# Kernel optimization log

Hardware: AMD Instinct MI355X
Metric: run time of the kernel (lower is better)

Reference implementation:

```python
import jax, jax.numpy as jnp
import numpy as np

ALPHA = 0.2      # LeakyReLU negative slope
NEG = -9e15     # mask fill value, as in pyGAT

B, N, NFEAT, NHID, NCLASS, NHEADS = 4, 2048, 128, 64, 32, 8


def setup_inputs() -> dict:
    key = jax.random.key(0)
    ks = jax.random.split(key, 8)
    x = jax.random.normal(ks[0], (B, N, NFEAT), dtype=jnp.float32)
    adj = jax.random.randint(ks[1], (B, N, N), 0, 2, dtype=jnp.int32)
    W = jax.random.normal(ks[2], (NHEADS, NFEAT, NHID), dtype=jnp.float32) * 0.1
    a1 = jax.random.normal(ks[3], (NHEADS, NHID), dtype=jnp.float32) * 0.1
    a2 = jax.random.normal(ks[4], (NHEADS, NHID), dtype=jnp.float32) * 0.1
    Wo = jax.random.normal(ks[5], (NHEADS * NHID, NCLASS), dtype=jnp.float32) * 0.1
    ao1 = jax.random.normal(ks[6], (NCLASS,), dtype=jnp.float32) * 0.1
    ao2 = jax.random.normal(ks[7], (NCLASS,), dtype=jnp.float32) * 0.1
    return {"x": x, "adj": adj, "W": W, "a1": a1, "a2": a2,
            "Wo": Wo, "ao1": ao1, "ao2": ao2}


def _gat_forward(x, adj, W, a1, a2, Wo, ao1, ao2):
    mask = adj > 0  # [B, N, N]
    # --- multi-head layer (concat=True) ---
    Wh = jnp.einsum('bnf,hfd->bhnd', x, W)          # [B,H,N,nhid]
    f1 = jnp.einsum('bhnd,hd->bhn', Wh, a1)          # Wh @ a[:nhid]
    f2 = jnp.einsum('bhnd,hd->bhn', Wh, a2)          # Wh @ a[nhid:]
    e = jax.nn.leaky_relu(f1[..., :, None] + f2[..., None, :], ALPHA)
    att = jax.nn.softmax(jnp.where(mask[:, None], e, NEG), axis=-1)
    h = jax.nn.elu(jnp.einsum('bhnm,bhmd->bhnd', att, Wh))  # [B,H,N,nhid]
    # torch.cat along dim=2: [B, N, H*nhid]
    h = jnp.transpose(h, (0, 2, 1, 3)).reshape(B, N, NHEADS * NHID)
    # (dropout layers are no-ops in eval mode)
    # --- output head (concat=False, no ELU) ---
    Wh2 = jnp.einsum('bnf,fc->bnc', h, Wo)           # [B,N,nclass]
    g1 = jnp.einsum('bnc,c->bn', Wh2, ao1)
    g2 = jnp.einsum('bnc,c->bn', Wh2, ao2)
    e2 = jax.nn.leaky_relu(g1[:, :, None] + g2[:, None, :], ALPHA)
    att2 = jax.nn.softmax(jnp.where(mask, e2, NEG), axis=-1)
    return jnp.einsum('bnm,bmc->bnc', att2, Wh2)     # [B,N,nclass]


def reference(x, adj, W, a1, a2, Wo, ao1, ao2):
    return _gat_forward(x, adj, W, a1, a2, Wo, ao1, ao2)
```

## Files before the change

kernel.cpp:

```cpp
#include <hip/hip_runtime.h>


typedef _Float16 half8  __attribute__((ext_vector_type(8)));
typedef _Float16 half2_ __attribute__((ext_vector_type(2)));
typedef float  float4_ __attribute__((ext_vector_type(4)));
typedef unsigned int uint4_ __attribute__((ext_vector_type(4)));

#if __has_builtin(__builtin_amdgcn_exp2f)
#define EXP2(x) __builtin_amdgcn_exp2f(x)
#else
#define EXP2(x) __expf((x) * 0.69314718055994531f)
#endif
#define LOG2E 1.44269504088896340f

static __device__ __forceinline__ unsigned pkh(float a, float b) {
#if __has_builtin(__builtin_amdgcn_cvt_pkrtz)
  return __builtin_bit_cast(unsigned, __builtin_amdgcn_cvt_pkrtz(a, b));
#else
  half2_ h = {(_Float16)a, (_Float16)b};
  return __builtin_bit_cast(unsigned, h);
#endif
}
static __device__ __forceinline__ unsigned short f2h(float f) {
  _Float16 h = (_Float16)f;
  return __builtin_bit_cast(unsigned short, h);
}

static __device__ __forceinline__ unsigned bitm(unsigned mb, int jj) {
#if __has_builtin(__builtin_amdgcn_sbfe)
  return (unsigned)__builtin_amdgcn_sbfe((int)mb, jj, 1);
#else
  return 0u - ((mb >> jj) & 1u);
#endif
}
static __device__ __forceinline__ unsigned pmask(unsigned s0, unsigned s1) {
  return __builtin_amdgcn_perm(s1, s0, 0x05040100u);
}
static __device__ __forceinline__ unsigned wmaxh(unsigned u, unsigned u2,
    unsigned pm, half2_ Ah, half2_ A2h) {
  half2_ p = Ah * __builtin_bit_cast(half2_, u);
  half2_ n = A2h * __builtin_bit_cast(half2_, u2);
  half2_ m = __builtin_elementwise_max(p, n);
  return __builtin_bit_cast(unsigned, m) & pm;
}

__global__ __launch_bounds__(256) void k_wfrag(
    const float* __restrict__ Wm, const float* __restrict__ Wo,
    unsigned short* __restrict__ Wf, unsigned short* __restrict__ WoF) {
  if (blockIdx.x < 32) {
    const int T = blockIdx.x * 256 + threadIdx.x;
    const int lane = T & 63;
    int r = T >> 6;
    const int nt = r & 3; r >>= 2;
    const int kstep = r & 3; r >>= 2;
    const int h = r;
    const int kk = kstep * 32 + (lane >> 4) * 8;
    const int n = nt * 16 + (lane & 15);
    const float* sp = Wm + h * 8192 + kk * 64 + n;
    unsigned short o[8];
    #pragma unroll
    for (int jj = 0; jj < 8; ++jj) o[jj] = f2h(sp[jj * 64]);
    *(uint4_*)(Wf + T * 8) = *(uint4_*)o;
  } else {
    const int T = (blockIdx.x - 32) * 256 + threadIdx.x;
    const int lane = T & 63;
    const int nt = (T >> 6) & 1, kstep = T >> 7;
    const int kk = kstep * 32 + (lane >> 4) * 8;
    const int n = nt * 16 + (lane & 15);
    unsigned short o[8];
    #pragma unroll
    for (int jj = 0; jj < 8; ++jj) o[jj] = f2h(Wo[(kk + jj) * 32 + n]);
    *(uint4_*)(WoF + T * 8) = *(uint4_*)o;
  }
}

__global__ __launch_bounds__(256) void k_front(
    const int* __restrict__ adj, unsigned long long* __restrict__ maskb,
    const float* __restrict__ x, const unsigned short* __restrict__ Wf,
    const float* __restrict__ a1, const float* __restrict__ a2,
    unsigned short* __restrict__ WhF, float* __restrict__ f1,
    unsigned short* __restrict__ Uv, unsigned short* __restrict__ U2v) {
  __shared__ float wsm[64 * 68];
  const int bx = blockIdx.x;
  const int t = threadIdx.x;
  if (bx >= 1024) {
    const int lane = t & 63, wid = t >> 6;
    const int s = lane & 15;
    const long long row0 = (long long)(bx - 1024) * 4;
    for (int rr = 0; rr < 4; ++rr) {
      const long long row = row0 + rr;
      const int4* src = (const int4*)(adj + row * 2048);
      #pragma unroll
      for (int c = 0; c < 2; ++c) {
        int4 v = src[c * 256 + t];
        unsigned nib = (v.x != 0 ? 1u : 0u) | (v.y != 0 ? 2u : 0u) |
                       (v.z != 0 ? 4u : 0u) | (v.w != 0 ? 8u : 0u);
        unsigned lo = (s < 8) ? (nib << (s * 4)) : 0u;
        unsigned hi = (s >= 8) ? (nib << ((s - 8) * 4)) : 0u;
        #pragma unroll
        for (int off = 1; off < 16; off <<= 1) {
          lo |= __shfl_xor(lo, off);
          hi |= __shfl_xor(hi, off);
        }
        if (s == 0) {
          const int word = c * 16 + wid * 4 + (lane >> 4);
          maskb[(((row >> 11) * 32 + word) << 11) + (row & 2047)] =
              ((unsigned long long)hi << 32) | (unsigned long long)lo;
        }
      }
    }
    return;
  }
  const int itile = bx & 31, bh = bx >> 5;
  const int b = bh >> 3, h = bh & 7;
  const int i0 = itile * 64;
  const int lane = t & 63, w = t >> 6;
  const int cl = lane & 15, q = lane >> 4;
  const float* xrow = x + ((long long)b * 2048 + i0 + w * 16 + cl) * 128;
  const unsigned short* wfh = Wf + h * 8192;
  float4_ acc0 = {0.f, 0.f, 0.f, 0.f}, acc1 = acc0, acc2 = acc0, acc3 = acc0;
  #pragma unroll
  for (int kstep = 0; kstep < 4; ++kstep) {
    const float* xp = xrow + kstep * 32 + q * 8;
    const float4 xa = *(const float4*)xp;
    const float4 xb = *(const float4*)(xp + 4);
    uint4_ ap;
    ap.x = pkh(xa.x, xa.y);
    ap.y = pkh(xa.z, xa.w);
    ap.z = pkh(xb.x, xb.y);
    ap.w = pkh(xb.z, xb.w);
    const half8 af = __builtin_bit_cast(half8, ap);
    const unsigned short* bp = wfh + kstep * 2048 + lane * 8;
    const half8 b0 = *(const half8*)(bp);
    const half8 b1 = *(const half8*)(bp + 512);
    const half8 b2 = *(const half8*)(bp + 1024);
    const half8 b3 = *(const half8*)(bp + 1536);
    acc0 = __builtin_amdgcn_mfma_f32_16x16x32_f16(af, b0, acc0, 0, 0, 0);
    acc1 = __builtin_amdgcn_mfma_f32_16x16x32_f16(af, b1, acc1, 0, 0, 0);
    acc2 = __builtin_amdgcn_mfma_f32_16x16x32_f16(af, b2, acc2, 0, 0, 0);
    acc3 = __builtin_amdgcn_mfma_f32_16x16x32_f16(af, b3, acc3, 0, 0, 0);
  }
  {
    float4_ accs[4] = {acc0, acc1, acc2, acc3};
    #pragma unroll
    for (int nt = 0; nt < 4; ++nt)
      #pragma unroll
      for (int reg = 0; reg < 4; ++reg)
        wsm[(w * 16 + q * 4 + reg) * 68 + nt * 16 + cl] = accs[nt][reg];
  }
  __syncthreads();
  {
    const int row = t >> 2, seg = t & 3;
    const float* wr = wsm + row * 68 + seg * 16;
    const float4* a1p = (const float4*)(a1 + h * 64 + seg * 16);
    const float4* a2p = (const float4*)(a2 + h * 64 + seg * 16);
    float p1 = 0.f, p2 = 0.f;
    #pragma unroll
    for (int u = 0; u < 4; ++u) {
      const float4 wv = *(const float4*)(wr + u * 4);
      const float4 v1 = a1p[u];
      const float4 v2 = a2p[u];
      p1 += wv.x * v1.x + wv.y * v1.y + wv.z * v1.z + wv.w * v1.w;
      p2 += wv.x * v2.x + wv.y * v2.y + wv.z * v2.z + wv.w * v2.w;
    }
    p1 += __shfl_xor(p1, 1); p1 += __shfl_xor(p1, 2);
    p2 += __shfl_xor(p2, 1); p2 += __shfl_xor(p2, 2);
    if (seg == 0) {
      f1[(long long)bh * 2048 + i0 + row] = p1 * LOG2E;
      const float s2 = p2 * LOG2E;
      Uv[(long long)bh * 2048 + i0 + row] = f2h(EXP2(s2));
      U2v[(long long)bh * 2048 + i0 + row] = f2h(EXP2(0.2f * s2));
    }
  }
  #pragma unroll
  for (int u = 0; u < 2; ++u) {
    const int idx = u * 256 + t;
    const int l2 = idx & 63, nt2 = (idx >> 6) & 3, ks2 = idx >> 8;
    const int jrow = ks2 * 32 + (l2 >> 4) * 8;
    const int d = nt2 * 16 + (l2 & 15);
    uint4_ o;
    o.x = pkh(wsm[(jrow + 0) * 68 + d], wsm[(jrow + 1) * 68 + d]);
    o.y = pkh(wsm[(jrow + 2) * 68 + d], wsm[(jrow + 3) * 68 + d]);
    o.z = pkh(wsm[(jrow + 4) * 68 + d], wsm[(jrow + 5) * 68 + d]);
    o.w = pkh(wsm[(jrow + 6) * 68 + d], wsm[(jrow + 7) * 68 + d]);
    const long long off = (long long)bh * 131072 + (long long)itile * 4096 +
                          ks2 * 2048 + nt2 * 512 + l2 * 8;
    *(uint4_*)(WhF + off) = o;
  }
}

__global__ __launch_bounds__(256) void k_attn1(
    const unsigned short* __restrict__ whf, const float* __restrict__ f1v,
    const unsigned short* __restrict__ Uv, const unsigned short* __restrict__ U2v,
    const unsigned long long* __restrict__ maskb, unsigned short* __restrict__ hA) {
  __shared__ __align__(16) unsigned short bsm[2][8192];
  const int bh = blockIdx.y, b = bh >> 3, hh = bh & 7;
  const int t = threadIdx.x;
  const int lane = t & 63, wid = t >> 6;
  const int cl = lane & 15, q = lane >> 4, qs = q * 8;
  const long long i_g = (long long)blockIdx.x * 64 + wid * 16 + cl;
  const float f1i = f1v[(long long)bh * 2048 + i_g];
  const float A = EXP2(f1i), A2 = EXP2(0.2f * f1i);
  const half2_ Ah = __builtin_bit_cast(half2_, pkh(A, A));
  const half2_ A2h = __builtin_bit_cast(half2_, pkh(A2, A2));
  const uint2* mT = (const uint2*)maskb;
  const long long mbase = (long long)b * 65536 + i_g;
  const unsigned short* whfb = whf + (long long)bh * 131072;
  const unsigned short* Ub  = Uv  + (long long)bh * 2048;
  const unsigned short* U2b = U2v + (long long)bh * 2048;
  const float4* gB = (const float4*)whfb;
  const half8 vones = {1.0f16, 1.0f16, 1.0f16, 1.0f16, 1.0f16, 1.0f16, 1.0f16, 1.0f16};
  {
    const float4 s0 = gB[t], s1 = gB[256 + t], s2 = gB[512 + t], s3 = gB[768 + t];
    float4* dp = (float4*)bsm[0] + t;
    dp[0] = s0; dp[256] = s1; dp[512] = s2; dp[768] = s3;
  }
  uint2 mw0_c = mT[mbase], mw1_c = mT[mbase + 2048];
  float4_ acc0 = {0.f, 0.f, 0.f, 0.f}, acc1 = acc0, acc2 = acc0, acc3 = acc0;
  float4_ accz = acc0;
  for (int s = 0; s < 16; ++s) {
    __syncthreads();
    const int sn = (s < 15) ? (s + 1) : 15;
    const float4* gp = gB + sn * 1024 + t;
    const float4 stn0 = gp[0], stn1 = gp[256], stn2 = gp[512], stn3 = gp[768];
    const uint2 mwA = mw0_c, mwB = mw1_c;
    mw0_c = mT[mbase + (long long)(sn * 2) * 2048];
    mw1_c = mT[mbase + (long long)(sn * 2 + 1) * 2048];
    const unsigned short* bsb = bsm[s & 1] + lane * 8;
    #pragma unroll
    for (int jc2 = 0; jc2 < 2; ++jc2) {
      const int jc = s * 2 + jc2;
      const uint2 mw = jc2 ? mwB : mwA;
      #pragma unroll
      for (int ks = 0; ks < 2; ++ks) {
        const uint4_ uv  = *(const uint4_*)(Ub  + jc * 64 + ks * 32 + qs);
        const uint4_ u2v = *(const uint4_*)(U2b + jc * 64 + ks * 32 + qs);
        const unsigned mb = (ks ? mw.y : mw.x) >> qs;
        const unsigned s0 = bitm(mb, 0), s1 = bitm(mb, 1), s2 = bitm(mb, 2),
                       s3 = bitm(mb, 3), s4 = bitm(mb, 4), s5 = bitm(mb, 5),
                       s6 = bitm(mb, 6), s7 = bitm(mb, 7);
        uint4_ pk;
        pk.x = wmaxh(uv.x, u2v.x, pmask(s0, s1), Ah, A2h);
        pk.y = wmaxh(uv.y, u2v.y, pmask(s2, s3), Ah, A2h);
        pk.z = wmaxh(uv.z, u2v.z, pmask(s4, s5), Ah, A2h);
        pk.w = wmaxh(uv.w, u2v.w, pmask(s6, s7), Ah, A2h);
        const half8 af = __builtin_bit_cast(half8, pk);
        const unsigned short* bp = bsb + (jc2 * 2 + ks) * 2048;
        const half8 b0 = *(const half8*)(bp);
        const half8 b1 = *(const half8*)(bp + 512);
        const half8 b2 = *(const half8*)(bp + 1024);
        const half8 b3 = *(const half8*)(bp + 1536);
        acc0 = __builtin_amdgcn_mfma_f32_16x16x32_f16(af, b0, acc0, 0, 0, 0);
        acc1 = __builtin_amdgcn_mfma_f32_16x16x32_f16(af, b1, acc1, 0, 0, 0);
        acc2 = __builtin_amdgcn_mfma_f32_16x16x32_f16(af, b2, acc2, 0, 0, 0);
        acc3 = __builtin_amdgcn_mfma_f32_16x16x32_f16(af, b3, acc3, 0, 0, 0);
        accz = __builtin_amdgcn_mfma_f32_16x16x32_f16(af, vones, accz, 0, 0, 0);
      }
    }
    if (s < 15) {
      float4* dp = (float4*)bsm[(s + 1) & 1] + t;
      dp[0] = stn0; dp[256] = stn1; dp[512] = stn2; dp[768] = stn3;
    }
  }
  __syncthreads();
  float* hs = (float*)bsm;
  {
    float4_ accs[4] = {acc0, acc1, acc2, acc3};
    #pragma unroll
    for (int reg = 0; reg < 4; ++reg) {
      const float rz = 1.f / accz[reg];
      #pragma unroll
      for (int nt = 0; nt < 4; ++nt) {
        float v = accs[nt][reg] * rz;
        v = (v > 0.f) ? v : (__expf(v) - 1.f);
        hs[(wid * 16 + q * 4 + reg) * 68 + nt * 16 + cl] = v;
      }
    }
  }
  __syncthreads();
  const int rtg0 = b * 128 + blockIdx.x * 4;
  #pragma unroll
  for (int u = 0; u < 2; ++u) {
    const int id = u * 256 + t;
    const int l2 = id & 63, ks2 = (id >> 6) & 1, rtile = id >> 7;
    const int rowl = rtile * 16 + (l2 & 15);
    const int d = ks2 * 32 + (l2 >> 4) * 8;
    const float* hp = hs + rowl * 68 + d;
    uint4_ o;
    o.x = pkh(hp[0], hp[1]); o.y = pkh(hp[2], hp[3]);
    o.z = pkh(hp[4], hp[5]); o.w = pkh(hp[6], hp[7]);
    const long long rt = rtg0 + rtile;
    const int kstep = hh * 2 + ks2;
    *(uint4_*)(hA + ((rt * 16 + kstep) * 64 + l2) * 8) = o;
  }
}

__global__ __launch_bounds__(128) void k_ogemm(
    const unsigned short* __restrict__ hA, const unsigned short* __restrict__ WoF,
    const float* __restrict__ ao1, const float* __restrict__ ao2,
    unsigned short* __restrict__ Wh2F, float* __restrict__ g1,
    unsigned short* __restrict__ gU, unsigned short* __restrict__ gU2) {
  __shared__ float w2s[32 * 36];
  const int t = threadIdx.x, lane = t & 63, wv = t >> 6;
  const int cl = lane & 15, q = lane >> 4;
  const long long rt = (long long)blockIdx.x * 2 + wv;
  float4_ acc0 = {0.f, 0.f, 0.f, 0.f}, acc1 = acc0;
  const unsigned short* ap = hA + rt * 8192 + lane * 8;
  const unsigned short* bp = WoF + lane * 8;
  #pragma unroll
  for (int kstep = 0; kstep < 16; ++kstep) {
    const half8 af = *(const half8*)(ap + kstep * 512);
    const half8 b0 = *(const half8*)(bp + kstep * 1024);
    const half8 b1 = *(const half8*)(bp + kstep * 1024 + 512);
    acc0 = __builtin_amdgcn_mfma_f32_16x16x32_f16(af, b0, acc0, 0, 0, 0);
    acc1 = __builtin_amdgcn_mfma_f32_16x16x32_f16(af, b1, acc1, 0, 0, 0);
  }
  const float o1a = ao1[cl], o1b = ao1[cl + 16];
  const float o2a = ao2[cl], o2b = ao2[cl + 16];
  #pragma unroll
  for (int reg = 0; reg < 4; ++reg) {
    const int rowl = wv * 16 + q * 4 + reg;
    w2s[rowl * 36 + cl] = acc0[reg];
    w2s[rowl * 36 + 16 + cl] = acc1[reg];
    float p1 = acc0[reg] * o1a + acc1[reg] * o1b;
    float p2 = acc0[reg] * o2a + acc1[reg] * o2b;
    p1 += __shfl_xor(p1, 1); p1 += __shfl_xor(p1, 2);
    p1 += __shfl_xor(p1, 4); p1 += __shfl_xor(p1, 8);
    p2 += __shfl_xor(p2, 1); p2 += __shfl_xor(p2, 2);
    p2 += __shfl_xor(p2, 4); p2 += __shfl_xor(p2, 8);
    if (cl == 0) {
      const long long row = (long long)blockIdx.x * 32 + rowl;
      g1[row] = p1 * LOG2E;
      const float s2 = p2 * LOG2E;
      gU[row]  = f2h(EXP2(s2));
      gU2[row] = f2h(EXP2(0.2f * s2));
    }
  }
  __syncthreads();
  {
    const int l2 = t & 63, nt2 = t >> 6;
    const int g = blockIdx.x >> 6, jc = (blockIdx.x >> 1) & 31, ks2 = blockIdx.x & 1;
    const int kb = (l2 >> 4) * 8, n = nt2 * 16 + (l2 & 15);
    uint4_ o;
    o.x = pkh(w2s[(kb + 0) * 36 + n], w2s[(kb + 1) * 36 + n]);
    o.y = pkh(w2s[(kb + 2) * 36 + n], w2s[(kb + 3) * 36 + n]);
    o.z = pkh(w2s[(kb + 4) * 36 + n], w2s[(kb + 5) * 36 + n]);
    o.w = pkh(w2s[(kb + 6) * 36 + n], w2s[(kb + 7) * 36 + n]);
    const long long off = (long long)g * 65536 + jc * 2048 + ks2 * 1024 +
                          nt2 * 512 + l2 * 8;
    *(uint4_*)(Wh2F + off) = o;
  }
}

__global__ __launch_bounds__(256) void k_attn2(
    const unsigned short* __restrict__ whf2, const float* __restrict__ g1v,
    const unsigned short* __restrict__ gU, const unsigned short* __restrict__ gU2,
    const unsigned long long* __restrict__ maskb, float* __restrict__ outp) {
  __shared__ float accs[4][16][33];
  __shared__ float zsh[64];
  const int b = blockIdx.y;
  const long long i0 = (long long)blockIdx.x * 16;
  const int t = threadIdx.x, lane = t & 63, wid = t >> 6;
  const int cl = lane & 15, q = lane >> 4;
  const float g1i = g1v[(long long)b * 2048 + i0 + cl];
  const float A = EXP2(g1i), A2 = EXP2(0.2f * g1i);
  const half2_ Ah = __builtin_bit_cast(half2_, pkh(A, A));
  const half2_ A2h = __builtin_bit_cast(half2_, pkh(A2, A2));
  const uint2* mT = (const uint2*)maskb;
  const int mrow = (int)(i0 + cl);
  const long long mbase = (long long)b * 65536 + mrow;
  const unsigned short* ub = gU + (long long)b * 2048;
  const unsigned short* u2b = gU2 + (long long)b * 2048;
  const unsigned short* wb = whf2 + (long long)b * 65536;
  const half8 vones = {1.0f16, 1.0f16, 1.0f16, 1.0f16, 1.0f16, 1.0f16, 1.0f16, 1.0f16};
  float4_ acc0 = {0.f, 0.f, 0.f, 0.f}, acc1 = acc0, accz = acc0;
  const int qs = q * 8;
  const int jc0 = wid * 8;
  uint2 mw_c = mT[mbase + (long long)jc0 * 2048];
  uint4_ ua_c  = *(const uint4_*)(ub  + jc0 * 64 + qs);
  uint4_ u2a_c = *(const uint4_*)(u2b + jc0 * 64 + qs);
  uint4_ ubn_c  = *(const uint4_*)(ub  + jc0 * 64 + 32 + qs);
  uint4_ u2b_c = *(const uint4_*)(u2b + jc0 * 64 + 32 + qs);
  for (int c8 = 0; c8 < 8; ++c8) {
    const int jc = jc0 + c8;
    const uint2 mw = mw_c;
    const uint4_ uA = ua_c, u2A = u2a_c, uB = ubn_c, u2B = u2b_c;
    {
      const int jn = jc + ((c8 < 7) ? 1 : 0);
      mw_c = mT[mbase + (long long)jn * 2048];
      ua_c  = *(const uint4_*)(ub  + jn * 64 + qs);
      u2a_c = *(const uint4_*)(u2b + jn * 64 + qs);
      ubn_c  = *(const uint4_*)(ub  + jn * 64 + 32 + qs);
      u2b_c = *(const uint4_*)(u2b + jn * 64 + 32 + qs);
    }
    const unsigned short* bb = wb + (jc * 2) * 1024 + lane * 8;
    #pragma unroll
    for (int ks = 0; ks < 2; ++ks) {
      const unsigned mb = (ks ? mw.y : mw.x) >> qs;
      const uint4_ uv  = ks ? uB : uA;
      const uint4_ u2v = ks ? u2B : u2A;
      const unsigned s0 = bitm(mb, 0), s1 = bitm(mb, 1), s2 = bitm(mb, 2),
                     s3 = bitm(mb, 3), s4 = bitm(mb, 4), s5 = bitm(mb, 5),
                     s6 = bitm(mb, 6), s7 = bitm(mb, 7);
      uint4_ pk;
      pk.x = wmaxh(uv.x, u2v.x, pmask(s0, s1), Ah, A2h);
      pk.y = wmaxh(uv.y, u2v.y, pmask(s2, s3), Ah, A2h);
      pk.z = wmaxh(uv.z, u2v.z, pmask(s4, s5), Ah, A2h);
      pk.w = wmaxh(uv.w, u2v.w, pmask(s6, s7), Ah, A2h);
      const half8 af = __builtin_bit_cast(half8, pk);
      const unsigned short* bk = bb + ks * 1024;
      const half8 b0 = *(const half8*)bk;
      const half8 b1 = *(const half8*)(bk + 512);
      acc0 = __builtin_amdgcn_mfma_f32_16x16x32_f16(af, b0, acc0, 0, 0, 0);
      acc1 = __builtin_amdgcn_mfma_f32_16x16x32_f16(af, b1, acc1, 0, 0, 0);
      accz = __builtin_amdgcn_mfma_f32_16x16x32_f16(af, vones, accz, 0, 0, 0);
    }
  }
  if (cl == 0) {
    #pragma unroll
    for (int reg = 0; reg < 4; ++reg) zsh[wid * 16 + q * 4 + reg] = accz[reg];
  }
  float4_ a01[2] = {acc0, acc1};
  #pragma unroll
  for (int nt = 0; nt < 2; ++nt)
    #pragma unroll
    for (int reg = 0; reg < 4; ++reg)
      accs[wid][q * 4 + reg][nt * 16 + cl] = a01[nt][reg];
  __syncthreads();
  #pragma unroll
  for (int r = 0; r < 2; ++r) {
    int o = r * 256 + t;
    int il = o >> 5, c = o & 31;
    float s = accs[0][il][c] + accs[1][il][c] + accs[2][il][c] + accs[3][il][c];
    float Z = zsh[il] + zsh[16 + il] + zsh[32 + il] + zsh[48 + il];
    outp[((long long)b * 2048 + i0 + il) * 32 + c] = s / Z;
  }
}

extern "C" void kernel_launch(void* const* d_in, const int* in_sizes, int n_in,
                              void* d_out, int out_size, void* d_ws, size_t ws_size,
                              hipStream_t stream) {
  const float* x   = (const float*)d_in[0];
  const int*   adj = (const int*)d_in[1];
  const float* W   = (const float*)d_in[2];
  const float* a1  = (const float*)d_in[3];
  const float* a2  = (const float*)d_in[4];
  const float* Wo  = (const float*)d_in[5];
  const float* ao1 = (const float*)d_in[6];
  const float* ao2 = (const float*)d_in[7];
  float* out = (float*)d_out;
  char* ws = (char*)d_ws;

  unsigned long long* maskb = (unsigned long long*)(ws + 0);
  unsigned short* Wf   = (unsigned short*)(ws + 2097152);
  unsigned short* WoF  = (unsigned short*)(ws + 2228224);
  unsigned short* WhF  = (unsigned short*)(ws + 18874368);
  float* f1   = (float*)(ws + 27262976);
  unsigned short* Uv  = (unsigned short*)(ws + 27525120);
  unsigned short* U2v = (unsigned short*)(ws + 27656192);
  unsigned short* hA  = (unsigned short*)(ws + 27787264);
  unsigned short* Wh2F = (unsigned short*)(ws + 45613056);
  float* g1   = (float*)(ws + 46137344);
  unsigned short* gU  = (unsigned short*)(ws + 46170112);
  unsigned short* gU2 = (unsigned short*)(ws + 46186496);

  hipLaunchKernelGGL(k_wfrag, dim3(40), dim3(256), 0, stream, W, Wo, Wf, WoF);
  hipLaunchKernelGGL(k_front, dim3(3072), dim3(256), 0, stream, adj, maskb,
                     x, Wf, a1, a2, WhF, f1, Uv, U2v);
  hipLaunchKernelGGL(k_attn1, dim3(32, 32), dim3(256), 0, stream, WhF, f1, Uv, U2v,
                     maskb, hA);
  hipLaunchKernelGGL(k_ogemm, dim3(256), dim3(128), 0, stream, hA, WoF, ao1, ao2,
                     Wh2F, g1, gU, gU2);
  hipLaunchKernelGGL(k_attn2, dim3(128, 4), dim3(256), 0, stream, Wh2F, g1, gU, gU2,
                     maskb, out);
}
```

Measured before the change: 171.9 us.

## Switch attention-1 to 32x32x16 MFMA with 2-wave blocks and LDS-staged U vectors

Rewrites the first attention kernel to use 32x32x16 f16 MFMA tiles instead of 16x16x32, so each wave covers 32 rows and the producer kernel writes WhF in a matching fragment layout. The block shrinks to 128 threads (two waves), each thread staging twice as many B-fragment loads per step. The U/U2 exponential vectors are now staged through LDS alongside the B tile rather than read from global per iteration. The output transposition uses a 67-float LDS stride, presumably to avoid bank conflicts. This aims to cut B-operand LDS reads per FLOP and global U traffic, at the cost of fewer threads per block and larger accumulators.

```diff
diff --git a/kernel.cpp b/kernel.cpp
--- a/kernel.cpp
+++ b/kernel.cpp
@@ -4,6 +4,7 @@
 typedef _Float16 half8  __attribute__((ext_vector_type(8)));
 typedef _Float16 half2_ __attribute__((ext_vector_type(2)));
 typedef float  float4_ __attribute__((ext_vector_type(4)));
+typedef float  floatx16 __attribute__((ext_vector_type(16)));
 typedef unsigned int uint4_ __attribute__((ext_vector_type(4)));
 
 #if __has_builtin(__builtin_amdgcn_exp2f)
@@ -175,117 +176,122 @@
   #pragma unroll
   for (int u = 0; u < 2; ++u) {
     const int idx = u * 256 + t;
-    const int l2 = idx & 63, nt2 = (idx >> 6) & 3, ks2 = idx >> 8;
-    const int jrow = ks2 * 32 + (l2 >> 4) * 8;
-    const int d = nt2 * 16 + (l2 & 15);
+    const int l2 = idx & 63, df = (idx >> 6) & 1, jbs = idx >> 7;
+    const int jrow = jbs * 16 + (l2 >> 5) * 8;
+    const int d = df * 32 + (l2 & 31);
     uint4_ o;
     o.x = pkh(wsm[(jrow + 0) * 68 + d], wsm[(jrow + 1) * 68 + d]);
     o.y = pkh(wsm[(jrow + 2) * 68 + d], wsm[(jrow + 3) * 68 + d]);
     o.z = pkh(wsm[(jrow + 4) * 68 + d], wsm[(jrow + 5) * 68 + d]);
     o.w = pkh(wsm[(jrow + 6) * 68 + d], wsm[(jrow + 7) * 68 + d]);
-    const long long off = (long long)bh * 131072 + (long long)itile * 4096 +
-                          ks2 * 2048 + nt2 * 512 + l2 * 8;
+    const long long off = (long long)bh * 131072 +
+                          ((long long)itile * 4 + jbs) * 1024 + df * 512 + l2 * 8;
     *(uint4_*)(WhF + off) = o;
   }
 }
 
-__global__ __launch_bounds__(256) void k_attn1(
+__global__ __launch_bounds__(128) void k_attn1(
     const unsigned short* __restrict__ whf, const float* __restrict__ f1v,
     const unsigned short* __restrict__ Uv, const unsigned short* __restrict__ U2v,
     const unsigned long long* __restrict__ maskb, unsigned short* __restrict__ hA) {
-  __shared__ __align__(16) unsigned short bsm[2][8192];
+  __shared__ __align__(16) unsigned short bsm[2][8448];
   const int bh = blockIdx.y, b = bh >> 3, hh = bh & 7;
   const int t = threadIdx.x;
-  const int lane = t & 63, wid = t >> 6;
-  const int cl = lane & 15, q = lane >> 4, qs = q * 8;
-  const long long i_g = (long long)blockIdx.x * 64 + wid * 16 + cl;
-  const float f1i = f1v[(long long)bh * 2048 + i_g];
+  const int lane = t & 63, w = t >> 6;
+  const int cl = lane & 31;
+  const int qh = lane >> 5, qs2 = qh * 8;
+  const long long rbase = (long long)bh * 2048;
+  const int row_l = blockIdx.x * 64 + w * 32 + cl;
+  const float f1i = f1v[rbase + row_l];
   const float A = EXP2(f1i), A2 = EXP2(0.2f * f1i);
   const half2_ Ah = __builtin_bit_cast(half2_, pkh(A, A));
   const half2_ A2h = __builtin_bit_cast(half2_, pkh(A2, A2));
   const uint2* mT = (const uint2*)maskb;
-  const long long mbase = (long long)b * 65536 + i_g;
+  const long long mbase = (long long)b * 65536 + row_l;
   const unsigned short* whfb = whf + (long long)bh * 131072;
-  const unsigned short* Ub  = Uv  + (long long)bh * 2048;
-  const unsigned short* U2b = U2v + (long long)bh * 2048;
   const float4* gB = (const float4*)whfb;
+  const unsigned* usrc = (const unsigned*)((t < 64 ? Uv : U2v) + rbase) + (t & 63);
   const half8 vones = {1.0f16, 1.0f16, 1.0f16, 1.0f16, 1.0f16, 1.0f16, 1.0f16, 1.0f16};
+  const floatx16 zero16 = {0.f, 0.f, 0.f, 0.f, 0.f, 0.f, 0.f, 0.f,
+                           0.f, 0.f, 0.f, 0.f, 0.f, 0.f, 0.f, 0.f};
+  floatx16 acc0 = zero16, acc1 = zero16, az = zero16;
   {
-    const float4 s0 = gB[t], s1 = gB[256 + t], s2 = gB[512 + t], s3 = gB[768 + t];
+    const float4* gp = gB + t;
+    float4 s0 = gp[0], s1 = gp[128], s2 = gp[256], s3 = gp[384];
+    float4 s4 = gp[512], s5 = gp[640], s6 = gp[768], s7 = gp[896];
+    const unsigned u0 = usrc[0];
     float4* dp = (float4*)bsm[0] + t;
-    dp[0] = s0; dp[256] = s1; dp[512] = s2; dp[768] = s3;
+    dp[0] = s0; dp[128] = s1; dp[256] = s2; dp[384] = s3;
+    dp[512] = s4; dp[640] = s5; dp[768] = s6; dp[896] = s7;
+    ((unsigned*)bsm[0])[4096 + t] = u0;
   }
   uint2 mw0_c = mT[mbase], mw1_c = mT[mbase + 2048];
-  float4_ acc0 = {0.f, 0.f, 0.f, 0.f}, acc1 = acc0, acc2 = acc0, acc3 = acc0;
-  float4_ accz = acc0;
   for (int s = 0; s < 16; ++s) {
     __syncthreads();
     const int sn = (s < 15) ? (s + 1) : 15;
-    const float4* gp = gB + sn * 1024 + t;
-    const float4 stn0 = gp[0], stn1 = gp[256], stn2 = gp[512], stn3 = gp[768];
+    float4 st0, st1, st2, st3, st4, st5, st6, st7;
+    {
+      const float4* gp = gB + sn * 1024 + t;
+      st0 = gp[0]; st1 = gp[128]; st2 = gp[256]; st3 = gp[384];
+      st4 = gp[512]; st5 = gp[640]; st6 = gp[768]; st7 = gp[896];
+    }
+    const unsigned ustg = usrc[sn * 64];
     const uint2 mwA = mw0_c, mwB = mw1_c;
     mw0_c = mT[mbase + (long long)(sn * 2) * 2048];
     mw1_c = mT[mbase + (long long)(sn * 2 + 1) * 2048];
-    const unsigned short* bsb = bsm[s & 1] + lane * 8;
-    #pragma unroll
-    for (int jc2 = 0; jc2 < 2; ++jc2) {
-      const int jc = s * 2 + jc2;
-      const uint2 mw = jc2 ? mwB : mwA;
-      #pragma unroll
-      for (int ks = 0; ks < 2; ++ks) {
-        const uint4_ uv  = *(const uint4_*)(Ub  + jc * 64 + ks * 32 + qs);
-        const uint4_ u2v = *(const uint4_*)(U2b + jc * 64 + ks * 32 + qs);
-        const unsigned mb = (ks ? mw.y : mw.x) >> qs;
-        const unsigned s0 = bitm(mb, 0), s1 = bitm(mb, 1), s2 = bitm(mb, 2),
-                       s3 = bitm(mb, 3), s4 = bitm(mb, 4), s5 = bitm(mb, 5),
-                       s6 = bitm(mb, 6), s7 = bitm(mb, 7);
-        uint4_ pk;
-        pk.x = wmaxh(uv.x, u2v.x, pmask(s0, s1), Ah, A2h);
-        pk.y = wmaxh(uv.y, u2v.y, pmask(s2, s3), Ah, A2h);
-        pk.z = wmaxh(uv.z, u2v.z, pmask(s4, s5), Ah, A2h);
-        pk.w = wmaxh(uv.w, u2v.w, pmask(s6, s7), Ah, A2h);
-        const half8 af = __builtin_bit_cast(half8, pk);
-        const unsigned short* bp = bsb + (jc2 * 2 + ks) * 2048;
-        const half8 b0 = *(const half8*)(bp);
-        const half8 b1 = *(const half8*)(bp + 512);
-        const half8 b2 = *(const half8*)(bp + 1024);
-        const half8 b3 = *(const half8*)(bp + 1536);
-        acc0 = __builtin_amdgcn_mfma_f32_16x16x32_f16(af, b0, acc0, 0, 0, 0);
-        acc1 = __builtin_amdgcn_mfma_f32_16x16x32_f16(af, b1, acc1, 0, 0, 0);
-        acc2 = __builtin_amdgcn_mfma_f32_16x16x32_f16(af, b2, acc2, 0, 0, 0);
-        acc3 = __builtin_amdgcn_mfma_f32_16x16x32_f16(af, b3, acc3, 0, 0, 0);
-        accz = __builtin_amdgcn_mfma_f32_16x16x32_f16(af, vones, accz, 0, 0, 0);
-      }
+    const unsigned short* bs = bsm[s & 1];
+    #pragma unroll
+    for (int ks = 0; ks < 8; ++ks) {
+      const uint2 mwu = (ks < 4) ? mwA : mwB;
+      const unsigned mword = (ks & 2) ? mwu.y : mwu.x;
+      const unsigned mb = mword >> (((ks & 1) << 4) + qs2);
+      const uint4_ uv  = *(const uint4_*)(bs + 8192 + ks * 16 + qs2);
+      const uint4_ u2v = *(const uint4_*)(bs + 8320 + ks * 16 + qs2);
+      const unsigned short* bp = bs + ks * 1024 + lane * 8;
+      const half8 b0 = *(const half8*)(bp);
+      const half8 b1 = *(const half8*)(bp + 512);
+      const unsigned s0 = bitm(mb, 0), s1 = bitm(mb, 1), s2 = bitm(mb, 2),
+                     s3 = bitm(mb, 3), s4 = bitm(mb, 4), s5 = bitm(mb, 5),
+                     s6 = bitm(mb, 6), s7 = bitm(mb, 7);
+      uint4_ pk;
+      pk.x = wmaxh(uv.x, u2v.x, pmask(s0, s1), Ah, A2h);
+      pk.y = wmaxh(uv.y, u2v.y, pmask(s2, s3), Ah, A2h);
+      pk.z = wmaxh(uv.z, u2v.z, pmask(s4, s5), Ah, A2h);
+      pk.w = wmaxh(uv.w, u2v.w, pmask(s6, s7), Ah, A2h);
+      const half8 af = __builtin_bit_cast(half8, pk);
+      acc0 = __builtin_amdgcn_mfma_f32_32x32x16_f16(af, b0, acc0, 0, 0, 0);
+      acc1 = __builtin_amdgcn_mfma_f32_32x32x16_f16(af, b1, acc1, 0, 0, 0);
+      az   = __builtin_amdgcn_mfma_f32_32x32x16_f16(af, vones, az, 0, 0, 0);
     }
     if (s < 15) {
       float4* dp = (float4*)bsm[(s + 1) & 1] + t;
-      dp[0] = stn0; dp[256] = stn1; dp[512] = stn2; dp[768] = stn3;
+      dp[0] = st0; dp[128] = st1; dp[256] = st2; dp[384] = st3;
+      dp[512] = st4; dp[640] = st5; dp[768] = st6; dp[896] = st7;
+      ((unsigned*)bsm[(s + 1) & 1])[4096 + t] = ustg;
     }
   }
   __syncthreads();
   float* hs = (float*)bsm;
-  {
-    float4_ accs[4] = {acc0, acc1, acc2, acc3};
-    #pragma unroll
-    for (int reg = 0; reg < 4; ++reg) {
-      const float rz = 1.f / accz[reg];
-      #pragma unroll
-      for (int nt = 0; nt < 4; ++nt) {
-        float v = accs[nt][reg] * rz;
-        v = (v > 0.f) ? v : (__expf(v) - 1.f);
-        hs[(wid * 16 + q * 4 + reg) * 68 + nt * 16 + cl] = v;
-      }
-    }
+  #pragma unroll
+  for (int reg = 0; reg < 16; ++reg) {
+    const int crow = (reg & 3) + 8 * (reg >> 2) + 4 * qh;
+    const float rz = 1.f / az[reg];
+    float v0 = acc0[reg] * rz;
+    v0 = (v0 > 0.f) ? v0 : (__expf(v0) - 1.f);
+    hs[(w * 32 + crow) * 67 + cl] = v0;
+    float v1 = acc1[reg] * rz;
+    v1 = (v1 > 0.f) ? v1 : (__expf(v1) - 1.f);
+    hs[(w * 32 + crow) * 67 + 32 + cl] = v1;
   }
   __syncthreads();
   const int rtg0 = b * 128 + blockIdx.x * 4;
   #pragma unroll
-  for (int u = 0; u < 2; ++u) {
-    const int id = u * 256 + t;
+  for (int u = 0; u < 4; ++u) {
+    const int id = u * 128 + t;
     const int l2 = id & 63, ks2 = (id >> 6) & 1, rtile = id >> 7;
     const int rowl = rtile * 16 + (l2 & 15);
     const int d = ks2 * 32 + (l2 >> 4) * 8;
-    const float* hp = hs + rowl * 68 + d;
+    const float* hp = hs + rowl * 67 + d;
     uint4_ o;
     o.x = pkh(hp[0], hp[1]); o.y = pkh(hp[2], hp[3]);
     o.z = pkh(hp[4], hp[5]); o.w = pkh(hp[6], hp[7]);
@@ -467,7 +473,7 @@
   hipLaunchKernelGGL(k_wfrag, dim3(40), dim3(256), 0, stream, W, Wo, Wf, WoF);
   hipLaunchKernelGGL(k_front, dim3(3072), dim3(256), 0, stream, adj, maskb,
                      x, Wf, a1, a2, WhF, f1, Uv, U2v);
-  hipLaunchKernelGGL(k_attn1, dim3(32, 32), dim3(256), 0, stream, WhF, f1, Uv, U2v,
+  hipLaunchKernelGGL(k_attn1, dim3(32, 32), dim3(128), 0, stream, WhF, f1, Uv, U2v,
                      maskb, hA);
   hipLaunchKernelGGL(k_ogemm, dim3(256), dim3(128), 0, stream, hA, WoF, ao1, ao2,
                      Wh2F, g1, gU, gU2);
```

New measurement: 168.3 us. -2.1%, faster.
